# Optimization experiments

Measured on AMD Instinct MI355X. Metric: run time of the kernel, lower is better.

The kernel has to match this reference:

```python
import jax, jax.numpy as jnp
import numpy as np

EPS = 1e-5  # torch LayerNorm default


def _ln(x, g, b):
    m = jnp.mean(x, axis=-1, keepdims=True)
    v = jnp.var(x, axis=-1, keepdims=True)
    return (x - m) * jax.lax.rsqrt(v + EPS) * g + b


def _attn(x, ctx, wq, wk, wv, wo, bo, num_heads):
    # weights stored [in, out]; equivalent to torch Linear (y = x @ W^T + b)
    B, T, _ = x.shape
    S = ctx.shape[1]
    E = wq.shape[1]
    hd = E // num_heads
    q = (x @ wq).reshape(B, T, num_heads, hd)
    k = (ctx @ wk).reshape(B, S, num_heads, hd)
    v = (ctx @ wv).reshape(B, S, num_heads, hd)
    scores = jnp.einsum('bthd,bshd->bhts', q, k) / np.sqrt(hd).astype(x.dtype)
    p = jax.nn.softmax(scores, axis=-1)
    o = jnp.einsum('bhts,bshd->bthd', p, v).reshape(B, T, E)
    return o @ wo + bo


def _ffn(x, w1, b1, w2, b2):
    h = jax.nn.gelu(x @ w1 + b1, approximate=False)  # torch nn.GELU default is exact
    return h @ w2 + b2  # Dropout(0.1) is identity in eval mode


def setup_inputs() -> dict:
    key = jax.random.key(0)
    H, CD, FF = 1024, 768, 4096
    ks = jax.random.split(key, 20)
    s = 0.02
    inp = {
        'x': jax.random.normal(ks[0], (4, 1024, H), jnp.float32),
        'context': jax.random.normal(ks[1], (4, 77, CD), jnp.float32),
        # self-attention params
        'sq_w': jax.random.normal(ks[2], (H, H), jnp.float32) * s,
        'sk_w': jax.random.normal(ks[3], (H, H), jnp.float32) * s,
        'sv_w': jax.random.normal(ks[4], (H, H), jnp.float32) * s,
        'so_w': jax.random.normal(ks[5], (H, H), jnp.float32) * s,
        'so_b': jnp.zeros((H,), jnp.float32),
        # cross-attention params
        'cq_w': jax.random.normal(ks[6], (H, H), jnp.float32) * s,
        'ck_w': jax.random.normal(ks[7], (CD, H), jnp.float32) * s,
        'cv_w': jax.random.normal(ks[8], (CD, H), jnp.float32) * s,
        'co_w': jax.random.normal(ks[9], (H, H), jnp.float32) * s,
        'co_b': jnp.zeros((H,), jnp.float32),
        # layer norms 1-4
        'n1_g': jnp.ones((H,), jnp.float32), 'n1_b': jnp.zeros((H,), jnp.float32),
        'n2_g': jnp.ones((H,), jnp.float32), 'n2_b': jnp.zeros((H,), jnp.float32),
        'n3_g': jnp.ones((H,), jnp.float32), 'n3_b': jnp.zeros((H,), jnp.float32),
        'n4_g': jnp.ones((H,), jnp.float32), 'n4_b': jnp.zeros((H,), jnp.float32),
        # FFNs
        'f1_w1': jax.random.normal(ks[10], (H, FF), jnp.float32) * s,
        'f1_b1': jnp.zeros((FF,), jnp.float32),
        'f1_w2': jax.random.normal(ks[11], (FF, H), jnp.float32) * s,
        'f1_b2': jnp.zeros((H,), jnp.float32),
        'f2_w1': jax.random.normal(ks[12], (H, FF), jnp.float32) * s,
        'f2_b1': jnp.zeros((FF,), jnp.float32),
        'f2_w2': jax.random.normal(ks[13], (FF, H), jnp.float32) * s,
        'f2_b2': jnp.zeros((H,), jnp.float32),
    }
    return inp


def reference(x, context,
              sq_w, sk_w, sv_w, so_w, so_b,
              cq_w, ck_w, cv_w, co_w, co_b,
              n1_g, n1_b, n2_g, n2_b, n3_g, n3_b, n4_g, n4_b,
              f1_w1, f1_b1, f1_w2, f1_b2,
              f2_w1, f2_b1, f2_w2, f2_b2):
    NUM_HEADS = 16
    # self-attention branch
    x = _attn(_ln(x, n1_g, n1_b), _ln(x, n1_g, n1_b), sq_w, sk_w, sv_w, so_w, so_b, NUM_HEADS) + x
    x = _ffn(_ln(x, n2_g, n2_b), f1_w1, f1_b1, f1_w2, f1_b2) + x
    # cross-attention branch
    x = _attn(_ln(x, n3_g, n3_b), context, cq_w, ck_w, cv_w, co_w, co_b, NUM_HEADS) + x
    x = _ffn(_ln(x, n4_g, n4_b), f2_w1, f2_b1, f2_w2, f2_b2) + x
    return x
```

## Files before the change

### kernel.cpp

```cpp
#include <hip/hip_runtime.h>
#include <cstdint>
#include <cstddef>

typedef unsigned short u16;
typedef __attribute__((ext_vector_type(8))) short short8;
typedef __attribute__((ext_vector_type(4))) float floatx4;

typedef const __attribute__((address_space(1))) void g_void;
typedef __attribute__((address_space(3))) void l_void;

__device__ __forceinline__ float b2f(u16 u) {
    union { unsigned int i; float f; } v; v.i = ((unsigned int)u) << 16; return v.f;
}
__device__ __forceinline__ u16 f2b(float f) {
    union { float f; unsigned int i; } v; v.f = f;
    unsigned int x = v.i;
    return (u16)((x + 0x7fffu + ((x >> 16) & 1u)) >> 16);
}
__device__ __forceinline__ float gelu_exact(float x) {
    return 0.5f * x * (1.0f + erff(x * 0.70710678118654752440f));
}

__global__ void sniff_kernel(const u16* __restrict__ x, int* __restrict__ flag) {
    int lane = threadIdx.x;
    int sane = 0;
    for (int i = lane * 2; i < 4096; i += 128) {
        int e = (x[i] >> 7) & 0xff;
        if (e >= 100 && e <= 140) sane++;
    }
#pragma unroll
    for (int off = 32; off; off >>= 1) sane += __shfl_xor(sane, off, 64);
    if (lane == 0) *flag = (sane * 2 >= 2048) ? 0 : 1;
}

__global__ __launch_bounds__(256) void cvt_x_kernel(const void* __restrict__ in,
                                                    float* __restrict__ out, int n4,
                                                    const int* __restrict__ flag) {
    int i = blockIdx.x * 256 + threadIdx.x;
    if (i >= n4) return;
    bool isf = (*flag != 0);
    float4 o;
    if (isf) {
        o = ((const float4*)in)[i];
    } else {
        uint2 w = ((const uint2*)in)[i];
        o.x = b2f((u16)(w.x & 0xffff)); o.y = b2f((u16)(w.x >> 16));
        o.z = b2f((u16)(w.y & 0xffff)); o.w = b2f((u16)(w.y >> 16));
    }
    ((float4*)out)[i] = o;
}

__global__ __launch_bounds__(256) void cvt_bf_kernel(const void* __restrict__ in,
                                                     u16* __restrict__ out, int n4,
                                                     const int* __restrict__ flag) {
    int i = blockIdx.x * 256 + threadIdx.x;
    if (i >= n4) return;
    bool isf = (*flag != 0);
    uint2 pk;
    if (isf) {
        float4 v = ((const float4*)in)[i];
        pk.x = (unsigned)f2b(v.x) | ((unsigned)f2b(v.y) << 16);
        pk.y = (unsigned)f2b(v.z) | ((unsigned)f2b(v.w) << 16);
    } else {
        pk = ((const uint2*)in)[i];
    }
    ((uint2*)out)[i] = pk;
}

struct TEnt { const void* src; u16* dst; int R, C, tiles_x, tiles; };
struct TPack { TEnt e[12]; };

__global__ __launch_bounds__(256) void transpose_batch_kernel(TPack p, const int* __restrict__ flag) {
    TEnt e = p.e[blockIdx.y];
    if ((int)blockIdx.x >= e.tiles) return;
    __shared__ u16 t[32][33];
    bool isf = (*flag != 0);
    int tx = threadIdx.x, ty = threadIdx.y;
    int c0 = (blockIdx.x % e.tiles_x) * 32;
    int r0 = (blockIdx.x / e.tiles_x) * 32;
#pragma unroll
    for (int i = 0; i < 4; i++) {
        size_t idx = (size_t)(r0 + ty + i * 8) * e.C + c0 + tx;
        t[ty + i * 8][tx] = isf ? f2b(((const float*)e.src)[idx]) : ((const u16*)e.src)[idx];
    }
    __syncthreads();
#pragma unroll
    for (int i = 0; i < 4; i++)
        e.dst[(size_t)(c0 + ty + i * 8) * e.R + r0 + tx] = t[tx][ty + i * 8];
}

__global__ __launch_bounds__(256) void ln_kernel(const float* __restrict__ x,
                                                 const void* __restrict__ g,
                                                 const void* __restrict__ bb,
                                                 u16* __restrict__ out,
                                                 const int* __restrict__ flag) {
    const int row = blockIdx.x;
    const int tid = threadIdx.x;
    const int lane = tid & 63, wave = tid >> 6;
    bool isf = (*flag != 0);
    size_t base = (size_t)row * 1024 + tid * 4;
    float4 xv = *(const float4*)(x + base);
    float s  = xv.x + xv.y + xv.z + xv.w;
    float s2 = xv.x * xv.x + xv.y * xv.y + xv.z * xv.z + xv.w * xv.w;
#pragma unroll
    for (int off = 32; off; off >>= 1) {
        s  += __shfl_xor(s, off, 64);
        s2 += __shfl_xor(s2, off, 64);
    }
    __shared__ float red[8];
    if (lane == 0) { red[wave] = s; red[4 + wave] = s2; }
    __syncthreads();
    s  = red[0] + red[1] + red[2] + red[3];
    s2 = red[4] + red[5] + red[6] + red[7];
    const float inv_n = 1.0f / 1024.0f;
    float mean = s * inv_n;
    float var  = s2 * inv_n - mean * mean;
    float rstd = rsqrtf(var + 1e-5f);
    float gv[4], bv[4];
    if (isf) {
        float4 gg = *(const float4*)((const float*)g + tid * 4);
        float4 bo = *(const float4*)((const float*)bb + tid * 4);
        gv[0] = gg.x; gv[1] = gg.y; gv[2] = gg.z; gv[3] = gg.w;
        bv[0] = bo.x; bv[1] = bo.y; bv[2] = bo.z; bv[3] = bo.w;
    } else {
        uint2 go = *(const uint2*)((const u16*)g + tid * 4);
        uint2 bo = *(const uint2*)((const u16*)bb + tid * 4);
        gv[0] = b2f((u16)(go.x & 0xffff)); gv[1] = b2f((u16)(go.x >> 16));
        gv[2] = b2f((u16)(go.y & 0xffff)); gv[3] = b2f((u16)(go.y >> 16));
        bv[0] = b2f((u16)(bo.x & 0xffff)); bv[1] = b2f((u16)(bo.x >> 16));
        bv[2] = b2f((u16)(bo.y & 0xffff)); bv[3] = b2f((u16)(bo.y >> 16));
    }
    float xa[4] = { xv.x, xv.y, xv.z, xv.w };
    u16 o[4];
#pragma unroll
    for (int j = 0; j < 4; j++)
        o[j] = f2b((xa[j] - mean) * rstd * gv[j] + bv[j]);
    uint2 pk;
    pk.x = (unsigned)o[0] | ((unsigned)o[1] << 16);
    pk.y = (unsigned)o[2] | ((unsigned)o[3] << 16);
    *(uint2*)(out + base) = pk;
}

template <int MODE, int MT, int NT, int MINW>
__global__ __launch_bounds__(256, MINW) void gemm_kernel(const u16* __restrict__ A,
                                                         const u16* __restrict__ BT,
                                                         const void* __restrict__ bias,
                                                         const float* __restrict__ res,
                                                         void* __restrict__ Cout,
                                                         int M, int N, int K,
                                                         const int* __restrict__ flag) {
    __shared__ __align__(16) u16 lsA[MT * 32 * 64];
    __shared__ __align__(16) u16 lsB[NT * 32 * 64];
    const int tid = threadIdx.x;
    const int lane = tid & 63;
    const int wave = tid >> 6;
    const int wm = (wave >> 1) * (MT * 16);
    const int wn = (wave & 1) * (NT * 16);
    const int bm = blockIdx.y * (MT * 32);
    const int bn = blockIdx.x * (NT * 32);
    const int l16 = lane & 15;
    const int lq = lane >> 4;
    const bool isf = (*flag != 0);

    floatx4 acc[MT][NT] = {};

    const int r_loc = tid >> 3;
    const int cb_log = ((tid & 7) - r_loc) & 7;
    const int gcol = cb_log * 8;

    const u16* gA[MT];
#pragma unroll
    for (int j = 0; j < MT; j++) {
        int rr = bm + j * 32 + r_loc; if (rr >= M) rr = M - 1;
        gA[j] = A + (size_t)rr * K + gcol;
    }
    const u16* gB[NT];
#pragma unroll
    for (int j = 0; j < NT; j++)
        gB[j] = BT + (size_t)(bn + j * 32 + r_loc) * K + gcol;

    for (int k0 = 0; k0 < K; k0 += 64) {
#pragma unroll
        for (int j = 0; j < MT; j++)
            __builtin_amdgcn_global_load_lds((g_void*)(gA[j] + k0),
                                             (l_void*)(lsA + j * 2048 + wave * 512), 16, 0, 0);
#pragma unroll
        for (int j = 0; j < NT; j++)
            __builtin_amdgcn_global_load_lds((g_void*)(gB[j] + k0),
                                             (l_void*)(lsB + j * 2048 + wave * 512), 16, 0, 0);
        __syncthreads();

#pragma unroll
        for (int ki = 0; ki < 2; ki++) {
            short8 af[MT], bf[NT];
#pragma unroll
            for (int mi = 0; mi < MT; mi++) {
                int ra = wm + mi * 16 + l16;
                af[mi] = *(const short8*)&lsA[ra * 64 + ((lq + ki * 4 + ra) & 7) * 8];
            }
#pragma unroll
            for (int ni = 0; ni < NT; ni++) {
                int rb = wn + ni * 16 + l16;
                bf[ni] = *(const short8*)&lsB[rb * 64 + ((lq + ki * 4 + rb) & 7) * 8];
            }
#pragma unroll
            for (int mi = 0; mi < MT; mi++)
#pragma unroll
                for (int ni = 0; ni < NT; ni++)
                    acc[mi][ni] = __builtin_amdgcn_mfma_f32_16x16x32_bf16(af[mi], bf[ni], acc[mi][ni], 0, 0, 0);
        }
        __syncthreads();
    }

#pragma unroll
    for (int mi = 0; mi < MT; mi++) {
#pragma unroll
        for (int ni = 0; ni < NT; ni++) {
            int col = bn + wn + ni * 16 + l16;
            float bv = 0.0f;
            if (bias) bv = isf ? ((const float*)bias)[col] : b2f(((const u16*)bias)[col]);
#pragma unroll
            for (int r = 0; r < 4; r++) {
                int row = bm + wm + mi * 16 + lq * 4 + r;
                if (row < M) {
                    float v = acc[mi][ni][r] + bv;
                    size_t idx = (size_t)row * N + col;
                    if (MODE == 1) v = gelu_exact(v);
                    if (MODE == 2 || MODE == 3) v += res[idx];
                    if (MODE == 2)       ((float*)Cout)[idx] = v;
                    else if (MODE == 3) { if (isf) ((float*)Cout)[idx] = v; else ((u16*)Cout)[idx] = f2b(v); }
                    else                 ((u16*)Cout)[idx] = f2b(v);
                }
            }
        }
    }
}

__global__ __launch_bounds__(256) void attn_mfma_kernel(const u16* __restrict__ q,
                                                        const u16* __restrict__ k,
                                                        const u16* __restrict__ v,
                                                        u16* __restrict__ o,
                                                        int T, int S, int ldq, int ldkv,
                                                        float cexp) {
    const int E = 1024;
    const int b = blockIdx.y >> 4, h = blockIdx.y & 15;
    const int tid = threadIdx.x, wave = tid >> 6, lane = tid & 63;
    const int l16 = lane & 15, lq = lane >> 4;

    __shared__ __align__(16) u16 Qs[64 * 64];
    __shared__ __align__(16) u16 Ks[64 * 64];
    __shared__ __align__(16) u16 Vt[64 * 72];
    __shared__ __align__(16) u16 Ps[4][16][72];

    const int q0 = blockIdx.x * 64;
    const int r8 = tid >> 3;
    const int cb_log = ((tid & 7) - r8) & 7;
    const int rv = tid >> 2, cv = (tid & 3) * 16;
    const int cbv = ((rv >> 3) ^ (tid & 3)) & 7;

#pragma unroll
    for (int j = 0; j < 2; j++) {
        int row = q0 + j * 32 + r8;
        __builtin_amdgcn_global_load_lds((g_void*)(q + (size_t)(b * T + row) * ldq + h * 64 + cb_log * 8),
                                         (l_void*)(Qs + j * 2048 + wave * 512), 16, 0, 0);
    }
    __syncthreads();

    const int qrow = wave * 16 + l16;
    short8 af0 = *(const short8*)&Qs[qrow * 64 + ((lq + qrow) & 7) * 8];
    short8 af1 = *(const short8*)&Qs[qrow * 64 + ((lq + 4 + qrow) & 7) * 8];

    float lsum[4] = { 0.f, 0.f, 0.f, 0.f };
    floatx4 oacc[4] = {};

    const int ntiles = (S + 63) >> 6;
    for (int t = 0; t < ntiles; t++) {
        const int s0 = t * 64;
        __syncthreads();
#pragma unroll
        for (int j = 0; j < 2; j++) {
            int srow = s0 + j * 32 + r8; if (srow >= S) srow = S - 1;
            __builtin_amdgcn_global_load_lds((g_void*)(k + (size_t)(b * S + srow) * ldkv + h * 64 + cb_log * 8),
                                             (l_void*)(Ks + j * 2048 + wave * 512), 16, 0, 0);
        }
        {
            int sr = s0 + rv; if (sr >= S) sr = S - 1;
            const u16* vsrc = v + (size_t)(b * S + sr) * ldkv + h * 64 + cv;
            uint4 v0 = *(const uint4*)vsrc;
            uint4 v1 = *(const uint4*)(vsrc + 8);
            const u16* vp = (const u16*)&v0;
#pragma unroll
            for (int j = 0; j < 8; j++)
                Vt[(cv + j) * 72 + cbv * 8 + (rv & 7)] = vp[j];
            vp = (const u16*)&v1;
#pragma unroll
            for (int j = 0; j < 8; j++)
                Vt[(cv + 8 + j) * 72 + cbv * 8 + (rv & 7)] = vp[j];
        }
        __syncthreads();

        floatx4 sc[4];
#pragma unroll
        for (int nt = 0; nt < 4; nt++) {
            int krow = nt * 16 + l16;
            short8 bf0 = *(const short8*)&Ks[krow * 64 + ((lq + krow) & 7) * 8];
            short8 bf1 = *(const short8*)&Ks[krow * 64 + ((lq + 4 + krow) & 7) * 8];
            floatx4 z = {};
            z = __builtin_amdgcn_mfma_f32_16x16x32_bf16(af0, bf0, z, 0, 0, 0);
            z = __builtin_amdgcn_mfma_f32_16x16x32_bf16(af1, bf1, z, 0, 0, 0);
            sc[nt] = z;
        }

        const bool tail = (s0 + 64 > S);
#pragma unroll
        for (int nt = 0; nt < 4; nt++) {
            bool colv = !tail || (s0 + nt * 16 + l16 < S);
#pragma unroll
            for (int r = 0; r < 4; r++) {
                float p = exp2f(sc[nt][r] * cexp);
                p = colv ? p : 0.0f;
                lsum[r] += p;
                Ps[wave][lq * 4 + r][nt * 16 + l16] = f2b(p);
            }
        }

        short8 av0 = *(const short8*)&Ps[wave][l16][lq * 8];
        short8 av1 = *(const short8*)&Ps[wave][l16][32 + lq * 8];

#pragma unroll
        for (int dt = 0; dt < 4; dt++) {
            int d = dt * 16 + l16;
            short8 bv0 = *(const short8*)&Vt[d * 72 + ((lq ^ dt) & 7) * 8];
            short8 bv1 = *(const short8*)&Vt[d * 72 + (((4 + lq) ^ dt) & 7) * 8];
            oacc[dt] = __builtin_amdgcn_mfma_f32_16x16x32_bf16(av0, bv0, oacc[dt], 0, 0, 0);
            oacc[dt] = __builtin_amdgcn_mfma_f32_16x16x32_bf16(av1, bv1, oacc[dt], 0, 0, 0);
        }
    }

#pragma unroll
    for (int r = 0; r < 4; r++) {
#pragma unroll
        for (int off = 1; off < 16; off <<= 1)
            lsum[r] += __shfl_xor(lsum[r], off, 64);
    }

#pragma unroll
    for (int r = 0; r < 4; r++) {
        float inv = 1.0f / lsum[r];
        int row = q0 + wave * 16 + lq * 4 + r;
        u16* dst = o + (size_t)(b * T + row) * E + h * 64 + l16;
#pragma unroll
        for (int dt = 0; dt < 4; dt++)
            dst[dt * 16] = f2b(oacc[dt][r] * inv);
    }
}

extern "C" void kernel_launch(void* const* d_in, const int* in_sizes, int n_in,
                              void* d_out, int out_size, void* d_ws, size_t ws_size,
                              hipStream_t stream) {
    const void* x_in = d_in[0];
    const void* ctx  = d_in[1];
    const void* sq_w = d_in[2];
    const void* sk_w = d_in[3];
    const void* sv_w = d_in[4];
    const void* so_w = d_in[5];
    const void* so_b = d_in[6];
    const void* cq_w = d_in[7];
    const void* ck_w = d_in[8];
    const void* cv_w = d_in[9];
    const void* co_w = d_in[10];
    const void* co_b = d_in[11];
    const void* n1_g = d_in[12];
    const void* n1_b = d_in[13];
    const void* n2_g = d_in[14];
    const void* n2_b = d_in[15];
    const void* n3_g = d_in[16];
    const void* n3_b = d_in[17];
    const void* n4_g = d_in[18];
    const void* n4_b = d_in[19];
    const void* f1_w1 = d_in[20];
    const void* f1_b1 = d_in[21];
    const void* f1_w2 = d_in[22];
    const void* f1_b2 = d_in[23];
    const void* f2_w1 = d_in[24];
    const void* f2_b1 = d_in[25];
    const void* f2_w2 = d_in[26];
    const void* f2_b2 = d_in[27];

    const int B = 4, T = 1024, H = 1024, FF = 4096, CD = 768, S = 77;
    const int BT_ = B * T;
    const int BS_ = B * S;

    char* ws = (char*)d_ws;
    size_t off = 0;
    auto alloc = [&](size_t bytes) { char* p = ws + off; off += (bytes + 255) & ~(size_t)255; return p; };
    int*   flag = (int*)alloc(256);
    u16*   ctxb = (u16*)alloc((size_t)BS_ * CD * 2);
    float* xcur = (float*)alloc((size_t)BT_ * H * 4);
    const size_t MEL = 1024 * 1024;
    u16* wqkv = (u16*)alloc(3 * MEL * 2);
    u16* wso  = (u16*)alloc(MEL * 2);
    u16* wcq  = (u16*)alloc(MEL * 2);
    u16* wckv = (u16*)alloc((size_t)2 * H * CD * 2);
    u16* wco  = (u16*)alloc(MEL * 2);
    u16* wf1a = (u16*)alloc((size_t)H * FF * 2);
    u16* wf1b = (u16*)alloc((size_t)H * FF * 2);
    u16* wf2a = (u16*)alloc((size_t)H * FF * 2);
    u16* wf2b = (u16*)alloc((size_t)H * FF * 2);
    u16* U    = (u16*)alloc((size_t)40 * 1024 * 1024);
    (void)ws_size; (void)n_in; (void)in_sizes; (void)out_size;

    const size_t AEL = (size_t)BT_ * H;
    u16* lnb  = U;
    u16* qkvb = U + AEL;
    u16* ob   = U + 4 * AEL;
    u16* hb   = U + AEL;
    u16* qb   = U + AEL;
    u16* kvb  = U + 2 * AEL;

    TPack tp;
    auto ent = [&](int i, const void* src, u16* dst, int R, int C) {
        tp.e[i] = TEnt{ src, dst, R, C, C / 32, (C / 32) * (R / 32) };
    };
    ent(0,  sq_w, wqkv,           H,  H);
    ent(1,  sk_w, wqkv + MEL,     H,  H);
    ent(2,  sv_w, wqkv + 2 * MEL, H,  H);
    ent(3,  so_w, wso,            H,  H);
    ent(4,  cq_w, wcq,            H,  H);
    ent(5,  ck_w, wckv,           CD, H);
    ent(6,  cv_w, wckv + (size_t)H * CD, CD, H);
    ent(7,  co_w, wco,            H,  H);
    ent(8,  f1_w1, wf1a,          H,  FF);
    ent(9,  f1_w2, wf1b,          FF, H);
    ent(10, f2_w1, wf2a,          H,  FF);
    ent(11, f2_w2, wf2b,          FF, H);

    const dim3 g_qkv(3072 / 128, BT_ / 128);
    const dim3 g_ff(FF / 128, BT_ / 128);
    const dim3 g_n1024(H / 64, BT_ / 64);
    const dim3 g_ckv(2048 / 64, (BS_ + 63) / 64);
    const dim3 attn_grid(T / 64, B * 16);
    const float cexp = 0.125f * 1.4426950408889634f;

    sniff_kernel<<<1, 64, 0, stream>>>((const u16*)x_in, flag);
    cvt_x_kernel<<<(BT_ * H / 4 + 255) / 256, 256, 0, stream>>>(x_in, xcur, BT_ * H / 4, flag);
    cvt_bf_kernel<<<(BS_ * CD / 4 + 255) / 256, 256, 0, stream>>>(ctx, ctxb, BS_ * CD / 4, flag);
    transpose_batch_kernel<<<dim3(4096, 12), dim3(32, 8), 0, stream>>>(tp, flag);

    ln_kernel<<<BT_, 256, 0, stream>>>(xcur, n1_g, n1_b, lnb, flag);
    gemm_kernel<0, 4, 4, 3><<<g_qkv, 256, 0, stream>>>(lnb, wqkv, nullptr, nullptr, qkvb, BT_, 3072, H, flag);
    attn_mfma_kernel<<<attn_grid, 256, 0, stream>>>(qkvb, qkvb + 1024, qkvb + 2048, ob, T, T, 3072, 3072, cexp);
    gemm_kernel<2, 2, 2, 6><<<g_n1024, 256, 0, stream>>>(ob, wso, so_b, xcur, xcur, BT_, H, H, flag);

    ln_kernel<<<BT_, 256, 0, stream>>>(xcur, n2_g, n2_b, lnb, flag);
    gemm_kernel<1, 4, 4, 3><<<g_ff, 256, 0, stream>>>(lnb, wf1a, f1_b1, nullptr, hb, BT_, FF, H, flag);
    gemm_kernel<2, 2, 2, 6><<<g_n1024, 256, 0, stream>>>(hb, wf1b, f1_b2, xcur, xcur, BT_, H, FF, flag);

    ln_kernel<<<BT_, 256, 0, stream>>>(xcur, n3_g, n3_b, lnb, flag);
    gemm_kernel<0, 2, 2, 6><<<g_n1024, 256, 0, stream>>>(lnb, wcq, nullptr, nullptr, qb, BT_, H, H, flag);
    gemm_kernel<0, 2, 2, 6><<<g_ckv, 256, 0, stream>>>(ctxb, wckv, nullptr, nullptr, kvb, BS_, 2048, CD, flag);
    attn_mfma_kernel<<<attn_grid, 256, 0, stream>>>(qb, kvb, kvb + 1024, ob, T, S, 1024, 2048, cexp);
    gemm_kernel<2, 2, 2, 6><<<g_n1024, 256, 0, stream>>>(ob, wco, co_b, xcur, xcur, BT_, H, H, flag);

    ln_kernel<<<BT_, 256, 0, stream>>>(xcur, n4_g, n4_b, lnb, flag);
    gemm_kernel<1, 4, 4, 3><<<g_ff, 256, 0, stream>>>(lnb, wf2a, f2_b1, nullptr, hb, BT_, FF, H, flag);
    gemm_kernel<3, 2, 2, 6><<<g_n1024, 256, 0, stream>>>(hb, wf2b, f2_b2, xcur, d_out, BT_, H, FF, flag);
}
```

Before: 635.2 us.

## Fuse input conversion into LayerNorm, add BK-templated GEMM, widen attention Q tile

Removes the separate fp32 conversion kernel for x by having the first LayerNorm read raw input and write the fp32 residual copy. Templates the GEMM on the K-tile depth and uses BK=128 with a lower occupancy hint for the N=1024 GEMMs, which halves the number of K-loop barriers per tile. Makes each attention block handle 128 query rows so K/V tiles staged in LDS are reused by twice as many rows. The cost is more LDS and registers per block, which lowers occupancy.

```diff
diff --git a/kernel.cpp b/kernel.cpp
--- a/kernel.cpp
+++ b/kernel.cpp
@@ -31,23 +31,6 @@
 #pragma unroll
     for (int off = 32; off; off >>= 1) sane += __shfl_xor(sane, off, 64);
     if (lane == 0) *flag = (sane * 2 >= 2048) ? 0 : 1;
-}
-
-__global__ __launch_bounds__(256) void cvt_x_kernel(const void* __restrict__ in,
-                                                    float* __restrict__ out, int n4,
-                                                    const int* __restrict__ flag) {
-    int i = blockIdx.x * 256 + threadIdx.x;
-    if (i >= n4) return;
-    bool isf = (*flag != 0);
-    float4 o;
-    if (isf) {
-        o = ((const float4*)in)[i];
-    } else {
-        uint2 w = ((const uint2*)in)[i];
-        o.x = b2f((u16)(w.x & 0xffff)); o.y = b2f((u16)(w.x >> 16));
-        o.z = b2f((u16)(w.y & 0xffff)); o.w = b2f((u16)(w.y >> 16));
-    }
-    ((float4*)out)[i] = o;
 }
 
 __global__ __launch_bounds__(256) void cvt_bf_kernel(const void* __restrict__ in,
@@ -89,17 +72,27 @@
         e.dst[(size_t)(c0 + ty + i * 8) * e.R + r0 + tx] = t[tx][ty + i * 8];
 }
 
-__global__ __launch_bounds__(256) void ln_kernel(const float* __restrict__ x,
+__global__ __launch_bounds__(256) void ln_kernel(const void* __restrict__ x,
+                                                 float* __restrict__ xout,
                                                  const void* __restrict__ g,
                                                  const void* __restrict__ bb,
                                                  u16* __restrict__ out,
-                                                 const int* __restrict__ flag) {
+                                                 const int* __restrict__ flag,
+                                                 int raw) {
     const int row = blockIdx.x;
     const int tid = threadIdx.x;
     const int lane = tid & 63, wave = tid >> 6;
     bool isf = (*flag != 0);
     size_t base = (size_t)row * 1024 + tid * 4;
-    float4 xv = *(const float4*)(x + base);
+    float4 xv;
+    if (raw && !isf) {
+        uint2 w = ((const uint2*)x)[base >> 2];
+        xv.x = b2f((u16)(w.x & 0xffff)); xv.y = b2f((u16)(w.x >> 16));
+        xv.z = b2f((u16)(w.y & 0xffff)); xv.w = b2f((u16)(w.y >> 16));
+    } else {
+        xv = ((const float4*)x)[base >> 2];
+    }
+    if (raw) ((float4*)xout)[base >> 2] = xv;
     float s  = xv.x + xv.y + xv.z + xv.w;
     float s2 = xv.x * xv.x + xv.y * xv.y + xv.z * xv.z + xv.w * xv.w;
 #pragma unroll
@@ -141,7 +134,7 @@
     *(uint2*)(out + base) = pk;
 }
 
-template <int MODE, int MT, int NT, int MINW>
+template <int MODE, int MT, int NT, int BK, int MINW>
 __global__ __launch_bounds__(256, MINW) void gemm_kernel(const u16* __restrict__ A,
                                                          const u16* __restrict__ BT,
                                                          const void* __restrict__ bias,
@@ -149,8 +142,12 @@
                                                          void* __restrict__ Cout,
                                                          int M, int N, int K,
                                                          const int* __restrict__ flag) {
-    __shared__ __align__(16) u16 lsA[MT * 32 * 64];
-    __shared__ __align__(16) u16 lsB[NT * 32 * 64];
+    constexpr int CB  = BK / 8;
+    constexpr int CBM = CB - 1;
+    constexpr int RPC = 256 / CB;
+    constexpr int CPG = 32 / RPC;
+    __shared__ __align__(16) u16 lsA[MT * 32 * BK];
+    __shared__ __align__(16) u16 lsB[NT * 32 * BK];
     const int tid = threadIdx.x;
     const int lane = tid & 63;
     const int wave = tid >> 6;
@@ -164,44 +161,54 @@
 
     floatx4 acc[MT][NT] = {};
 
-    const int r_loc = tid >> 3;
-    const int cb_log = ((tid & 7) - r_loc) & 7;
+    const int r_in = tid / CB;
+    const int cb_log = ((tid & CBM) - r_in) & CBM;
     const int gcol = cb_log * 8;
 
-    const u16* gA[MT];
-#pragma unroll
-    for (int j = 0; j < MT; j++) {
-        int rr = bm + j * 32 + r_loc; if (rr >= M) rr = M - 1;
-        gA[j] = A + (size_t)rr * K + gcol;
-    }
-    const u16* gB[NT];
+    const u16* gA[MT * CPG];
+#pragma unroll
+    for (int j = 0; j < MT; j++)
+#pragma unroll
+        for (int c = 0; c < CPG; c++) {
+            int rr = bm + j * 32 + c * RPC + r_in; if (rr >= M) rr = M - 1;
+            gA[j * CPG + c] = A + (size_t)rr * K + gcol;
+        }
+    const u16* gB[NT * CPG];
 #pragma unroll
     for (int j = 0; j < NT; j++)
-        gB[j] = BT + (size_t)(bn + j * 32 + r_loc) * K + gcol;
-
-    for (int k0 = 0; k0 < K; k0 += 64) {
+#pragma unroll
+        for (int c = 0; c < CPG; c++) {
+            int rr = bn + j * 32 + c * RPC + r_in; if (rr >= N) rr = N - 1;
+            gB[j * CPG + c] = BT + (size_t)rr * K + gcol;
+        }
+
+    for (int k0 = 0; k0 < K; k0 += BK) {
 #pragma unroll
         for (int j = 0; j < MT; j++)
-            __builtin_amdgcn_global_load_lds((g_void*)(gA[j] + k0),
-                                             (l_void*)(lsA + j * 2048 + wave * 512), 16, 0, 0);
+#pragma unroll
+            for (int c = 0; c < CPG; c++)
+                __builtin_amdgcn_global_load_lds((g_void*)(gA[j * CPG + c] + k0),
+                                                 (l_void*)(lsA + (j * 32 + c * RPC) * BK + tid * 8), 16, 0, 0);
 #pragma unroll
         for (int j = 0; j < NT; j++)
-            __builtin_amdgcn_global_load_lds((g_void*)(gB[j] + k0),
-                                             (l_void*)(lsB + j * 2048 + wave * 512), 16, 0, 0);
+#pragma unroll
+            for (int c = 0; c < CPG; c++)
+                __builtin_amdgcn_global_load_lds((g_void*)(gB[j * CPG + c] + k0),
+                                                 (l_void*)(lsB + (j * 32 + c * RPC) * BK + tid * 8), 16, 0, 0);
         __syncthreads();
 
 #pragma unroll
-        for (int ki = 0; ki < 2; ki++) {
+        for (int ki = 0; ki < BK / 32; ki++) {
             short8 af[MT], bf[NT];
 #pragma unroll
             for (int mi = 0; mi < MT; mi++) {
                 int ra = wm + mi * 16 + l16;
-                af[mi] = *(const short8*)&lsA[ra * 64 + ((lq + ki * 4 + ra) & 7) * 8];
+                af[mi] = *(const short8*)&lsA[ra * BK + ((ki * 4 + lq + ra) & CBM) * 8];
             }
 #pragma unroll
             for (int ni = 0; ni < NT; ni++) {
                 int rb = wn + ni * 16 + l16;
-                bf[ni] = *(const short8*)&lsB[rb * 64 + ((lq + ki * 4 + rb) & 7) * 8];
+                bf[ni] = *(const short8*)&lsB[rb * BK + ((ki * 4 + lq + rb) & CBM) * 8];
             }
 #pragma unroll
             for (int mi = 0; mi < MT; mi++)
@@ -236,42 +243,46 @@
     }
 }
 
-__global__ __launch_bounds__(256) void attn_mfma_kernel(const u16* __restrict__ q,
-                                                        const u16* __restrict__ k,
-                                                        const u16* __restrict__ v,
-                                                        u16* __restrict__ o,
-                                                        int T, int S, int ldq, int ldkv,
-                                                        float cexp) {
+__global__ __launch_bounds__(256, 2) void attn_mfma_kernel(const u16* __restrict__ q,
+                                                           const u16* __restrict__ k,
+                                                           const u16* __restrict__ v,
+                                                           u16* __restrict__ o,
+                                                           int T, int S, int ldq, int ldkv,
+                                                           float cexp) {
     const int E = 1024;
     const int b = blockIdx.y >> 4, h = blockIdx.y & 15;
     const int tid = threadIdx.x, wave = tid >> 6, lane = tid & 63;
     const int l16 = lane & 15, lq = lane >> 4;
 
-    __shared__ __align__(16) u16 Qs[64 * 64];
+    __shared__ __align__(16) u16 Qs[128 * 64];
     __shared__ __align__(16) u16 Ks[64 * 64];
     __shared__ __align__(16) u16 Vt[64 * 72];
-    __shared__ __align__(16) u16 Ps[4][16][72];
-
-    const int q0 = blockIdx.x * 64;
+    __shared__ __align__(16) u16 Ps[4][16 * 72];
+
+    const int q0 = blockIdx.x * 128;
     const int r8 = tid >> 3;
     const int cb_log = ((tid & 7) - r8) & 7;
     const int rv = tid >> 2, cv = (tid & 3) * 16;
     const int cbv = ((rv >> 3) ^ (tid & 3)) & 7;
 
 #pragma unroll
-    for (int j = 0; j < 2; j++) {
+    for (int j = 0; j < 4; j++) {
         int row = q0 + j * 32 + r8;
         __builtin_amdgcn_global_load_lds((g_void*)(q + (size_t)(b * T + row) * ldq + h * 64 + cb_log * 8),
-                                         (l_void*)(Qs + j * 2048 + wave * 512), 16, 0, 0);
+                                         (l_void*)(Qs + j * 2048 + tid * 8), 16, 0, 0);
     }
     __syncthreads();
 
-    const int qrow = wave * 16 + l16;
-    short8 af0 = *(const short8*)&Qs[qrow * 64 + ((lq + qrow) & 7) * 8];
-    short8 af1 = *(const short8*)&Qs[qrow * 64 + ((lq + 4 + qrow) & 7) * 8];
-
-    float lsum[4] = { 0.f, 0.f, 0.f, 0.f };
-    floatx4 oacc[4] = {};
+    short8 af[2][2];
+#pragma unroll
+    for (int j = 0; j < 2; j++) {
+        int qr = j * 64 + wave * 16 + l16;
+        af[j][0] = *(const short8*)&Qs[qr * 64 + ((lq + qr) & 7) * 8];
+        af[j][1] = *(const short8*)&Qs[qr * 64 + ((lq + 4 + qr) & 7) * 8];
+    }
+
+    float lsum[2][4] = {};
+    floatx4 oacc[2][4] = {};
 
     const int ntiles = (S + 63) >> 6;
     for (int t = 0; t < ntiles; t++) {
@@ -281,7 +292,7 @@
         for (int j = 0; j < 2; j++) {
             int srow = s0 + j * 32 + r8; if (srow >= S) srow = S - 1;
             __builtin_amdgcn_global_load_lds((g_void*)(k + (size_t)(b * S + srow) * ldkv + h * 64 + cb_log * 8),
-                                             (l_void*)(Ks + j * 2048 + wave * 512), 16, 0, 0);
+                                             (l_void*)(Ks + j * 2048 + tid * 8), 16, 0, 0);
         }
         {
             int sr = s0 + rv; if (sr >= S) sr = S - 1;
@@ -299,60 +310,64 @@
         }
         __syncthreads();
 
-        floatx4 sc[4];
-#pragma unroll
-        for (int nt = 0; nt < 4; nt++) {
-            int krow = nt * 16 + l16;
-            short8 bf0 = *(const short8*)&Ks[krow * 64 + ((lq + krow) & 7) * 8];
-            short8 bf1 = *(const short8*)&Ks[krow * 64 + ((lq + 4 + krow) & 7) * 8];
-            floatx4 z = {};
-            z = __builtin_amdgcn_mfma_f32_16x16x32_bf16(af0, bf0, z, 0, 0, 0);
-            z = __builtin_amdgcn_mfma_f32_16x16x32_bf16(af1, bf1, z, 0, 0, 0);
-            sc[nt] = z;
-        }
-
         const bool tail = (s0 + 64 > S);
 #pragma unroll
-        for (int nt = 0; nt < 4; nt++) {
-            bool colv = !tail || (s0 + nt * 16 + l16 < S);
-#pragma unroll
-            for (int r = 0; r < 4; r++) {
-                float p = exp2f(sc[nt][r] * cexp);
-                p = colv ? p : 0.0f;
-                lsum[r] += p;
-                Ps[wave][lq * 4 + r][nt * 16 + l16] = f2b(p);
-            }
-        }
-
-        short8 av0 = *(const short8*)&Ps[wave][l16][lq * 8];
-        short8 av1 = *(const short8*)&Ps[wave][l16][32 + lq * 8];
-
-#pragma unroll
-        for (int dt = 0; dt < 4; dt++) {
-            int d = dt * 16 + l16;
-            short8 bv0 = *(const short8*)&Vt[d * 72 + ((lq ^ dt) & 7) * 8];
-            short8 bv1 = *(const short8*)&Vt[d * 72 + (((4 + lq) ^ dt) & 7) * 8];
-            oacc[dt] = __builtin_amdgcn_mfma_f32_16x16x32_bf16(av0, bv0, oacc[dt], 0, 0, 0);
-            oacc[dt] = __builtin_amdgcn_mfma_f32_16x16x32_bf16(av1, bv1, oacc[dt], 0, 0, 0);
-        }
-    }
-
-#pragma unroll
-    for (int r = 0; r < 4; r++) {
-#pragma unroll
-        for (int off = 1; off < 16; off <<= 1)
-            lsum[r] += __shfl_xor(lsum[r], off, 64);
-    }
-
-#pragma unroll
-    for (int r = 0; r < 4; r++) {
-        float inv = 1.0f / lsum[r];
-        int row = q0 + wave * 16 + lq * 4 + r;
-        u16* dst = o + (size_t)(b * T + row) * E + h * 64 + l16;
-#pragma unroll
-        for (int dt = 0; dt < 4; dt++)
-            dst[dt * 16] = f2b(oacc[dt][r] * inv);
-    }
+        for (int j = 0; j < 2; j++) {
+            floatx4 sc[4];
+#pragma unroll
+            for (int nt = 0; nt < 4; nt++) {
+                int krow = nt * 16 + l16;
+                short8 bf0 = *(const short8*)&Ks[krow * 64 + ((lq + krow) & 7) * 8];
+                short8 bf1 = *(const short8*)&Ks[krow * 64 + ((lq + 4 + krow) & 7) * 8];
+                floatx4 z = {};
+                z = __builtin_amdgcn_mfma_f32_16x16x32_bf16(af[j][0], bf0, z, 0, 0, 0);
+                z = __builtin_amdgcn_mfma_f32_16x16x32_bf16(af[j][1], bf1, z, 0, 0, 0);
+                sc[nt] = z;
+            }
+#pragma unroll
+            for (int nt = 0; nt < 4; nt++) {
+                bool colv = !tail || (s0 + nt * 16 + l16 < S);
+#pragma unroll
+                for (int r = 0; r < 4; r++) {
+                    float p = exp2f(sc[nt][r] * cexp);
+                    p = colv ? p : 0.0f;
+                    lsum[j][r] += p;
+                    Ps[wave][(lq * 4 + r) * 72 + nt * 16 + l16] = f2b(p);
+                }
+            }
+            short8 av0 = *(const short8*)&Ps[wave][l16 * 72 + lq * 8];
+            short8 av1 = *(const short8*)&Ps[wave][l16 * 72 + 32 + lq * 8];
+#pragma unroll
+            for (int dt = 0; dt < 4; dt++) {
+                int d = dt * 16 + l16;
+                short8 bv0 = *(const short8*)&Vt[d * 72 + ((lq ^ dt) & 7) * 8];
+                short8 bv1 = *(const short8*)&Vt[d * 72 + (((4 + lq) ^ dt) & 7) * 8];
+                oacc[j][dt] = __builtin_amdgcn_mfma_f32_16x16x32_bf16(av0, bv0, oacc[j][dt], 0, 0, 0);
+                oacc[j][dt] = __builtin_amdgcn_mfma_f32_16x16x32_bf16(av1, bv1, oacc[j][dt], 0, 0, 0);
+            }
+        }
+    }
+
+#pragma unroll
+    for (int j = 0; j < 2; j++)
+#pragma unroll
+        for (int r = 0; r < 4; r++) {
+#pragma unroll
+            for (int off = 1; off < 16; off <<= 1)
+                lsum[j][r] += __shfl_xor(lsum[j][r], off, 64);
+        }
+
+#pragma unroll
+    for (int j = 0; j < 2; j++)
+#pragma unroll
+        for (int r = 0; r < 4; r++) {
+            float inv = 1.0f / lsum[j][r];
+            int row = q0 + j * 64 + wave * 16 + lq * 4 + r;
+            u16* dst = o + (size_t)(b * T + row) * E + h * 64 + l16;
+#pragma unroll
+            for (int dt = 0; dt < 4; dt++)
+                dst[dt * 16] = f2b(oacc[j][dt][r] * inv);
+        }
 }
 
 extern "C" void kernel_launch(void* const* d_in, const int* in_sizes, int n_in,
@@ -439,30 +454,29 @@
     const dim3 g_ff(FF / 128, BT_ / 128);
     const dim3 g_n1024(H / 64, BT_ / 64);
     const dim3 g_ckv(2048 / 64, (BS_ + 63) / 64);
-    const dim3 attn_grid(T / 64, B * 16);
+    const dim3 attn_grid(T / 128, B * 16);
     const float cexp = 0.125f * 1.4426950408889634f;
 
     sniff_kernel<<<1, 64, 0, stream>>>((const u16*)x_in, flag);
-    cvt_x_kernel<<<(BT_ * H / 4 + 255) / 256, 256, 0, stream>>>(x_in, xcur, BT_ * H / 4, flag);
     cvt_bf_kernel<<<(BS_ * CD / 4 + 255) / 256, 256, 0, stream>>>(ctx, ctxb, BS_ * CD / 4, flag);
     transpose_batch_kernel<<<dim3(4096, 12), dim3(32, 8), 0, stream>>>(tp, flag);
 
-    ln_kernel<<<BT_, 256, 0, stream>>>(xcur, n1_g, n1_b, lnb, flag);
-    gemm_kernel<0, 4, 4, 3><<<g_qkv, 256, 0, stream>>>(lnb, wqkv, nullptr, nullptr, qkvb, BT_, 3072, H, flag);
+    ln_kernel<<<BT_, 256, 0, stream>>>(x_in, xcur, n1_g, n1_b, lnb, flag, 1);
+    gemm_kernel<0, 4, 4, 64, 3><<<g_qkv, 256, 0, stream>>>(lnb, wqkv, nullptr, nullptr, qkvb, BT_, 3072, H, flag);
     attn_mfma_kernel<<<attn_grid, 256, 0, stream>>>(qkvb, qkvb + 1024, qkvb + 2048, ob, T, T, 3072, 3072, cexp);
-    gemm_kernel<2, 2, 2, 6><<<g_n1024, 256, 0, stream>>>(ob, wso, so_b, xcur, xcur, BT_, H, H, flag);
-
-    ln_kernel<<<BT_, 256, 0, stream>>>(xcur, n2_g, n2_b, lnb, flag);
-    gemm_kernel<1, 4, 4, 3><<<g_ff, 256, 0, stream>>>(lnb, wf1a, f1_b1, nullptr, hb, BT_, FF, H, flag);
-    gemm_kernel<2, 2, 2, 6><<<g_n1024, 256, 0, stream>>>(hb, wf1b, f1_b2, xcur, xcur, BT_, H, FF, flag);
-
-    ln_kernel<<<BT_, 256, 0, stream>>>(xcur, n3_g, n3_b, lnb, flag);
-    gemm_kernel<0, 2, 2, 6><<<g_n1024, 256, 0, stream>>>(lnb, wcq, nullptr, nullptr, qb, BT_, H, H, flag);
-    gemm_kernel<0, 2, 2, 6><<<g_ckv, 256, 0, stream>>>(ctxb, wckv, nullptr, nullptr, kvb, BS_, 2048, CD, flag);
+    gemm_kernel<2, 2, 2, 128, 4><<<g_n1024, 256, 0, stream>>>(ob, wso, so_b, xcur, xcur, BT_, H, H, flag);
+
+    ln_kernel<<<BT_, 256, 0, stream>>>(xcur, nullptr, n2_g, n2_b, lnb, flag, 0);
+    gemm_kernel<1, 4, 4, 64, 3><<<g_ff, 256, 0, stream>>>(lnb, wf1a, f1_b1, nullptr, hb, BT_, FF, H, flag);
+    gemm_kernel<2, 2, 2, 128, 4><<<g_n1024, 256, 0, stream>>>(hb, wf1b, f1_b2, xcur, xcur, BT_, H, FF, flag);
+
+    ln_kernel<<<BT_, 256, 0, stream>>>(xcur, nullptr, n3_g, n3_b, lnb, flag, 0);
+    gemm_kernel<0, 2, 2, 128, 4><<<g_n1024, 256, 0, stream>>>(lnb, wcq, nullptr, nullptr, qb, BT_, H, H, flag);
+    gemm_kernel<0, 2, 2, 128, 4><<<g_ckv, 256, 0, stream>>>(ctxb, wckv, nullptr, nullptr, kvb, BS_, 2048, CD, flag);
     attn_mfma_kernel<<<attn_grid, 256, 0, stream>>>(qb, kvb, kvb + 1024, ob, T, S, 1024, 2048, cexp);
-    gemm_kernel<2, 2, 2, 6><<<g_n1024, 256, 0, stream>>>(ob, wco, co_b, xcur, xcur, BT_, H, H, flag);
-
-    ln_kernel<<<BT_, 256, 0, stream>>>(xcur, n4_g, n4_b, lnb, flag);
-    gemm_kernel<1, 4, 4, 3><<<g_ff, 256, 0, stream>>>(lnb, wf2a, f2_b1, nullptr, hb, BT_, FF, H, flag);
-    gemm_kernel<3, 2, 2, 6><<<g_n1024, 256, 0, stream>>>(hb, wf2b, f2_b2, xcur, d_out, BT_, H, FF, flag);
-}
+    gemm_kernel<2, 2, 2, 128, 4><<<g_n1024, 256, 0, stream>>>(ob, wco, co_b, xcur, xcur, BT_, H, H, flag);
+
+    ln_kernel<<<BT_, 256, 0, stream>>>(xcur, nullptr, n4_g, n4_b, lnb, flag, 0);
+    gemm_kernel<1, 4, 4, 64, 3><<<g_ff, 256, 0, stream>>>(lnb, wf2a, f2_b1, nullptr, hb, BT_, FF, H, flag);
+    gemm_kernel<3, 2, 2, 128, 4><<<g_n1024, 256, 0, stream>>>(hb, wf2b, f2_b2, xcur, d_out, BT_, H, FF, flag);
+}
```

After: 630.6 us. About the same (-0.7%).
